# Performance work log

Measured on AMD Instinct MI355X. Metric: run time of the kernel, lower is better.

The kernel has to match this reference:

```python
import jax, jax.numpy as jnp
import numpy as np

B, T, I, H = 4096, 128, 32, 64


def _u(key, shape, bound):
    return jax.random.uniform(key, shape, jnp.float32, -bound, bound)


def setup_inputs() -> dict:
    key = jax.random.key(0)
    ks = jax.random.split(key, 14)
    bound = 1.0 / np.sqrt(H)  # torch LSTM/Linear default init scale
    inp = {
        "x": jax.random.normal(ks[0], (B, T, I), jnp.float32),
        "Wih0": _u(ks[1], (4 * H, I), bound),
        "Whh0": _u(ks[2], (4 * H, H), bound),
        "bih0": _u(ks[3], (4 * H,), bound),
        "bhh0": _u(ks[4], (4 * H,), bound),
        "Wih1": _u(ks[5], (4 * H, H), bound),
        "Whh1": _u(ks[6], (4 * H, H), bound),
        "bih1": _u(ks[7], (4 * H,), bound),
        "bhh1": _u(ks[8], (4 * H,), bound),
        "Wc1": _u(ks[9], (32, H), 1.0 / np.sqrt(H)),
        "bc1": _u(ks[10], (32,), 1.0 / np.sqrt(H)),
        "Wc2": _u(ks[11], (1, 32), 1.0 / np.sqrt(32)),
        "bc2": _u(ks[12], (1,), 1.0 / np.sqrt(32)),
    }
    return inp


def lstm_layer(x_tbi, Wih, Whh, bih, bhh):
    """x_tbi: [T, B, in]. Returns (all hidden [T,B,H], final hidden [B,H]).
    PyTorch gate order: i, f, g, o."""
    b = x_tbi.shape[1]
    h0 = jnp.zeros((b, Whh.shape[1]), x_tbi.dtype)
    c0 = jnp.zeros_like(h0)
    # precompute input projections for all timesteps in one big GEMM
    xproj = jnp.einsum('tbi,gi->tbg', x_tbi, Wih) + (bih + bhh)

    def step(carry, xp_t):
        h, c = carry
        gates = xp_t + h @ Whh.T  # [B, 4H]
        i, f, g, o = jnp.split(gates, 4, axis=-1)
        c = jax.nn.sigmoid(f) * c + jax.nn.sigmoid(i) * jnp.tanh(g)
        h = jax.nn.sigmoid(o) * jnp.tanh(c)
        return (h, c), h

    (hT, _), hs = jax.lax.scan(step, (h0, c0), xproj)
    return hs, hT


def reference(x, Wih0, Whh0, bih0, bhh0, Wih1, Whh1, bih1, bhh1, Wc1, bc1, Wc2, bc2):
    x_tbi = jnp.transpose(x, (1, 0, 2))  # [T, B, I]
    hs0, _ = lstm_layer(x_tbi, Wih0, Whh0, bih0, bhh0)
    # dropout between layers is identity in eval mode
    _, hT = lstm_layer(hs0, Wih1, Whh1, bih1, bhh1)  # h_n[-1]: [B, H]
    hidden = jax.nn.relu(hT @ Wc1.T + bc1)  # [B, 32]; classifier dropout = identity (eval)
    out = hidden @ Wc2.T + bc2  # [B, 1]
    return out.squeeze(-1)  # [B]
```

## Files before the change

kernel.cpp:

```cpp
#include <hip/hip_runtime.h>


#define TT 128
#define II 32
#define HH 64

typedef _Float16 half8 __attribute__((ext_vector_type(8)));
typedef float floatx4 __attribute__((ext_vector_type(4)));

#define LOG2E 1.4426950408889634f

__device__ __forceinline__ half8 load_w_frag(const float* __restrict__ W, int n, int K, int k0) {
    const float* p = W + (size_t)n * K + k0;
    float4 a = *(const float4*)p;
    float4 b = *(const float4*)(p + 4);
    half8 h;
    h[0] = (_Float16)a.x; h[1] = (_Float16)a.y; h[2] = (_Float16)a.z; h[3] = (_Float16)a.w;
    h[4] = (_Float16)b.x; h[5] = (_Float16)b.y; h[6] = (_Float16)b.z; h[7] = (_Float16)b.w;
    return h;
}

__device__ __forceinline__ float sig_tanh(float a, float b) {
    float bb = fminf(fmaxf(b, -15.f), 15.f);
    float u  = __builtin_amdgcn_exp2f(bb * (2.0f * LOG2E));
    float v  = __builtin_amdgcn_exp2f(-a * LOG2E);
    float num = u - 1.0f;
    float d1  = u + 1.0f;
    float den = fmaf(v, d1, d1);
    return num * __builtin_amdgcn_rcpf(den);
}

__device__ __forceinline__ float fsig(float x) {
    return __builtin_amdgcn_rcpf(1.0f + __builtin_amdgcn_exp2f(-x * LOG2E));
}

__global__ __launch_bounds__(512, 2) void lstm_fused(
    const float* __restrict__ x,
    const float* __restrict__ Wih0, const float* __restrict__ Whh0,
    const float* __restrict__ bih0, const float* __restrict__ bhh0,
    const float* __restrict__ Wih1, const float* __restrict__ Whh1,
    const float* __restrict__ bih1, const float* __restrict__ bhh1,
    const float* __restrict__ Wc1, const float* __restrict__ bc1,
    const float* __restrict__ Wc2, const float* __restrict__ bc2,
    float* __restrict__ out)
{
    __shared__ __align__(16) _Float16 xs[2][16][40];
    __shared__ __align__(16) _Float16 h0s[2][16][72];
    __shared__ __align__(16) _Float16 h1s[2][16][72];
    __shared__ __align__(16) float h1f[16][68];
    __shared__ float hid[16][32];

    const int tid  = threadIdx.x;
    const int wid  = tid >> 6;
    const int w4   = wid & 3;
    const bool isL0 = (wid < 4);
    const int lane = tid & 63;
    const int q  = lane >> 4;
    const int lr = lane & 15;
    const int b0 = blockIdx.x * 16;

    half8 bx0[4], bh0[4][2];
    half8 bi1[4][2], bh1[4][2];
    float biasv[4];
    if (isL0) {
        #pragma unroll
        for (int g = 0; g < 4; ++g) {
            int n = (w4 + 4 * g) * 16 + lr;
            bx0[g]    = load_w_frag(Wih0, n, 32, q * 8);
            bh0[g][0] = load_w_frag(Whh0, n, 64, q * 8);
            bh0[g][1] = load_w_frag(Whh0, n, 64, 32 + q * 8);
            biasv[g]  = bih0[n] + bhh0[n];
        }
    } else {
        #pragma unroll
        for (int g = 0; g < 4; ++g) {
            int n = (w4 + 4 * g) * 16 + lr;
            bi1[g][0] = load_w_frag(Wih1, n, 64, q * 8);
            bi1[g][1] = load_w_frag(Wih1, n, 64, 32 + q * 8);
            bh1[g][0] = load_w_frag(Whh1, n, 64, q * 8);
            bh1[g][1] = load_w_frag(Whh1, n, 64, 32 + q * 8);
            biasv[g]  = bih1[n] + bhh1[n];
        }
    }

    for (int i = tid; i < 2 * 16 * 72; i += 512) {
        ((_Float16*)h0s)[i] = (_Float16)0.0f;
        ((_Float16*)h1s)[i] = (_Float16)0.0f;
    }

    float cr[4] = {0.f, 0.f, 0.f, 0.f};

    const int xm = (tid >> 4) & 15;
    const int xf = (tid & 15) * 2;
    const float* xrow = x + ((size_t)(b0 + xm) * TT) * II + xf;
    float2 xbuf = {0.f, 0.f};
    if (isL0) {
        float2 x0 = *(const float2*)(xrow);
        xs[0][xm][xf]     = (_Float16)x0.x;
        xs[0][xm][xf + 1] = (_Float16)x0.y;
        if (TT > 1) xbuf = *(const float2*)(xrow + 1 * II);
    }

    for (int k = 0; k <= TT; ++k) {
        __syncthreads();

        const int rd = (k + 1) & 1;
        const int wr = k & 1;
        const bool doL0 = isL0 && (k < TT);
        const bool doL1 = (!isL0) && (k >= 1);
        float hnew[4];
        float2 xnew = xbuf;

        if (doL0) {
            half8 xfrag = *(const half8*)&xs[wr][lr][q * 8];
            half8 h0a   = *(const half8*)&h0s[rd][lr][q * 8];
            half8 h0b   = *(const half8*)&h0s[rd][lr][32 + q * 8];
            if (k + 2 < TT) xnew = *(const float2*)(xrow + (size_t)(k + 2) * II);
            floatx4 a0[4];
            #pragma unroll
            for (int g = 0; g < 4; ++g) {
                floatx4 acc = {biasv[g], biasv[g], biasv[g], biasv[g]};
                acc = __builtin_amdgcn_mfma_f32_16x16x32_f16(xfrag, bx0[g],    acc, 0, 0, 0);
                acc = __builtin_amdgcn_mfma_f32_16x16x32_f16(h0a,   bh0[g][0], acc, 0, 0, 0);
                acc = __builtin_amdgcn_mfma_f32_16x16x32_f16(h0b,   bh0[g][1], acc, 0, 0, 0);
                a0[g] = acc;
            }
            #pragma unroll
            for (int r = 0; r < 4; ++r) {
                float sf = fsig(a0[1][r]);
                float c  = fmaf(sf, cr[r], sig_tanh(a0[0][r], a0[2][r]));
                cr[r] = c;
                hnew[r] = sig_tanh(a0[3][r], c);
            }
        }
        if (doL1) {
            half8 g0a = *(const half8*)&h0s[rd][lr][q * 8];
            half8 g0b = *(const half8*)&h0s[rd][lr][32 + q * 8];
            half8 h1a = *(const half8*)&h1s[rd][lr][q * 8];
            half8 h1b = *(const half8*)&h1s[rd][lr][32 + q * 8];
            floatx4 a1[4];
            #pragma unroll
            for (int g = 0; g < 4; ++g) {
                floatx4 acc = {biasv[g], biasv[g], biasv[g], biasv[g]};
                acc = __builtin_amdgcn_mfma_f32_16x16x32_f16(g0a, bi1[g][0], acc, 0, 0, 0);
                acc = __builtin_amdgcn_mfma_f32_16x16x32_f16(g0b, bi1[g][1], acc, 0, 0, 0);
                acc = __builtin_amdgcn_mfma_f32_16x16x32_f16(h1a, bh1[g][0], acc, 0, 0, 0);
                acc = __builtin_amdgcn_mfma_f32_16x16x32_f16(h1b, bh1[g][1], acc, 0, 0, 0);
                a1[g] = acc;
            }
            #pragma unroll
            for (int r = 0; r < 4; ++r) {
                float sf = fsig(a1[1][r]);
                float c  = fmaf(sf, cr[r], sig_tanh(a1[0][r], a1[2][r]));
                cr[r] = c;
                hnew[r] = sig_tanh(a1[3][r], c);
            }
        }

        if (doL0) {
            #pragma unroll
            for (int r = 0; r < 4; ++r)
                h0s[wr][q * 4 + r][w4 * 16 + lr] = (_Float16)hnew[r];
            if (k + 1 < TT) {
                xs[rd][xm][xf]     = (_Float16)xbuf.x;
                xs[rd][xm][xf + 1] = (_Float16)xbuf.y;
            }
            xbuf = xnew;
        }
        if (doL1) {
            if (k == TT) {
                #pragma unroll
                for (int r = 0; r < 4; ++r)
                    h1f[q * 4 + r][w4 * 16 + lr] = hnew[r];
            } else {
                #pragma unroll
                for (int r = 0; r < 4; ++r)
                    h1s[wr][q * 4 + r][w4 * 16 + lr] = (_Float16)hnew[r];
            }
        }
    }
    __syncthreads();

    if (tid < 256) {
        int m = tid >> 4;
        int u = (tid & 15) * 2;
        float a = bc1[u], b = bc1[u + 1];
        const float* w0 = Wc1 + u * 64;
        const float* w1 = Wc1 + (u + 1) * 64;
        #pragma unroll 8
        for (int kk = 0; kk < 64; ++kk) {
            float hv = h1f[m][kk];
            a += hv * w0[kk];
            b += hv * w1[kk];
        }
        hid[m][u]     = fmaxf(a, 0.f);
        hid[m][u + 1] = fmaxf(b, 0.f);
    }
    __syncthreads();
    if (tid < 16) {
        float o = bc2[0];
        #pragma unroll
        for (int u = 0; u < 32; ++u) o += hid[tid][u] * Wc2[u];
        out[b0 + tid] = o;
    }
}

extern "C" void kernel_launch(void* const* d_in, const int* in_sizes, int n_in,
                              void* d_out, int out_size, void* d_ws, size_t ws_size,
                              hipStream_t stream) {
    (void)in_sizes; (void)n_in; (void)d_ws; (void)ws_size; (void)out_size;
    const float* x    = (const float*)d_in[0];
    const float* Wih0 = (const float*)d_in[1];
    const float* Whh0 = (const float*)d_in[2];
    const float* bih0 = (const float*)d_in[3];
    const float* bhh0 = (const float*)d_in[4];
    const float* Wih1 = (const float*)d_in[5];
    const float* Whh1 = (const float*)d_in[6];
    const float* bih1 = (const float*)d_in[7];
    const float* bhh1 = (const float*)d_in[8];
    const float* Wc1  = (const float*)d_in[9];
    const float* bc1  = (const float*)d_in[10];
    const float* Wc2  = (const float*)d_in[11];
    const float* bc2  = (const float*)d_in[12];
    lstm_fused<<<dim3(256), dim3(512), 0, stream>>>(
        x, Wih0, Whh0, bih0, bhh0, Wih1, Whh1, bih1, bhh1, Wc1, bc1, Wc2, bc2,
        (float*)d_out);
}
```

Before: 206.0 us.

## Load x fragments directly into registers per lane, drop shared x staging

```diff
diff --git a/kernel.cpp b/kernel.cpp
--- a/kernel.cpp
+++ b/kernel.cpp
@@ -20,16 +20,25 @@
     return h;
 }
 
-__device__ __forceinline__ float sig_tanh(float a, float b) {
-    float bb = fminf(fmaxf(b, -15.f), 15.f);
-    float u  = __builtin_amdgcn_exp2f(bb * (2.0f * LOG2E));
+__device__ __forceinline__ half8 cvt_frag(float4 a, float4 b) {
+    half8 h;
+    h[0] = (_Float16)a.x; h[1] = (_Float16)a.y; h[2] = (_Float16)a.z; h[3] = (_Float16)a.w;
+    h[4] = (_Float16)b.x; h[5] = (_Float16)b.y; h[6] = (_Float16)b.z; h[7] = (_Float16)b.w;
+    return h;
+}
+
+__device__ __forceinline__ float sig_tanh_nc(float a, float b) {
+    float u  = __builtin_amdgcn_exp2f(b * (2.0f * LOG2E));
     float v  = __builtin_amdgcn_exp2f(-a * LOG2E);
     float num = u - 1.0f;
     float d1  = u + 1.0f;
     float den = fmaf(v, d1, d1);
     return num * __builtin_amdgcn_rcpf(den);
 }
-
+__device__ __forceinline__ float sig_tanh_cl(float a, float b) {
+    float bb = fminf(fmaxf(b, -15.f), 15.f);
+    return sig_tanh_nc(a, bb);
+}
 __device__ __forceinline__ float fsig(float x) {
     return __builtin_amdgcn_rcpf(1.0f + __builtin_amdgcn_exp2f(-x * LOG2E));
 }
@@ -44,7 +53,6 @@
     const float* __restrict__ Wc2, const float* __restrict__ bc2,
     float* __restrict__ out)
 {
-    __shared__ __align__(16) _Float16 xs[2][16][40];
     __shared__ __align__(16) _Float16 h0s[2][16][72];
     __shared__ __align__(16) _Float16 h1s[2][16][72];
     __shared__ __align__(16) float h1f[16][68];
@@ -90,17 +98,18 @@
 
     float cr[4] = {0.f, 0.f, 0.f, 0.f};
 
-    const int xm = (tid >> 4) & 15;
-    const int xf = (tid & 15) * 2;
-    const float* xrow = x + ((size_t)(b0 + xm) * TT) * II + xf;
-    float2 xbuf = {0.f, 0.f};
+    const float* xlane = x + ((size_t)(b0 + lr) * TT) * II + q * 8;
+    half8 xfrag_cur;
+    float4 xra, xrb;
     if (isL0) {
-        float2 x0 = *(const float2*)(xrow);
-        xs[0][xm][xf]     = (_Float16)x0.x;
-        xs[0][xm][xf + 1] = (_Float16)x0.y;
-        if (TT > 1) xbuf = *(const float2*)(xrow + 1 * II);
-    }
-
+        float4 a0 = *(const float4*)(xlane);
+        float4 b0f = *(const float4*)(xlane + 4);
+        xfrag_cur = cvt_frag(a0, b0f);
+        xra = *(const float4*)(xlane + II);
+        xrb = *(const float4*)(xlane + II + 4);
+    }
+
+    #pragma unroll 2
     for (int k = 0; k <= TT; ++k) {
         __syncthreads();
 
@@ -109,28 +118,30 @@
         const bool doL0 = isL0 && (k < TT);
         const bool doL1 = (!isL0) && (k >= 1);
         float hnew[4];
-        float2 xnew = xbuf;
 
         if (doL0) {
-            half8 xfrag = *(const half8*)&xs[wr][lr][q * 8];
-            half8 h0a   = *(const half8*)&h0s[rd][lr][q * 8];
-            half8 h0b   = *(const half8*)&h0s[rd][lr][32 + q * 8];
-            if (k + 2 < TT) xnew = *(const float2*)(xrow + (size_t)(k + 2) * II);
+            half8 h0a = *(const half8*)&h0s[rd][lr][q * 8];
+            half8 h0b = *(const half8*)&h0s[rd][lr][32 + q * 8];
+            half8 xfrag_nxt = cvt_frag(xra, xrb);
+            int t2 = (k + 2 < TT) ? (k + 2) : (TT - 1);
+            xra = *(const float4*)(xlane + (size_t)t2 * II);
+            xrb = *(const float4*)(xlane + (size_t)t2 * II + 4);
             floatx4 a0[4];
             #pragma unroll
             for (int g = 0; g < 4; ++g) {
                 floatx4 acc = {biasv[g], biasv[g], biasv[g], biasv[g]};
-                acc = __builtin_amdgcn_mfma_f32_16x16x32_f16(xfrag, bx0[g],    acc, 0, 0, 0);
-                acc = __builtin_amdgcn_mfma_f32_16x16x32_f16(h0a,   bh0[g][0], acc, 0, 0, 0);
-                acc = __builtin_amdgcn_mfma_f32_16x16x32_f16(h0b,   bh0[g][1], acc, 0, 0, 0);
+                acc = __builtin_amdgcn_mfma_f32_16x16x32_f16(xfrag_cur, bx0[g],    acc, 0, 0, 0);
+                acc = __builtin_amdgcn_mfma_f32_16x16x32_f16(h0a,       bh0[g][0], acc, 0, 0, 0);
+                acc = __builtin_amdgcn_mfma_f32_16x16x32_f16(h0b,       bh0[g][1], acc, 0, 0, 0);
                 a0[g] = acc;
             }
+            xfrag_cur = xfrag_nxt;
             #pragma unroll
             for (int r = 0; r < 4; ++r) {
                 float sf = fsig(a0[1][r]);
-                float c  = fmaf(sf, cr[r], sig_tanh(a0[0][r], a0[2][r]));
+                float c  = fmaf(sf, cr[r], sig_tanh_nc(a0[0][r], a0[2][r]));
                 cr[r] = c;
-                hnew[r] = sig_tanh(a0[3][r], c);
+                hnew[r] = sig_tanh_cl(a0[3][r], c);
             }
         }
         if (doL1) {
@@ -151,9 +162,9 @@
             #pragma unroll
             for (int r = 0; r < 4; ++r) {
                 float sf = fsig(a1[1][r]);
-                float c  = fmaf(sf, cr[r], sig_tanh(a1[0][r], a1[2][r]));
+                float c  = fmaf(sf, cr[r], sig_tanh_nc(a1[0][r], a1[2][r]));
                 cr[r] = c;
-                hnew[r] = sig_tanh(a1[3][r], c);
+                hnew[r] = sig_tanh_cl(a1[3][r], c);
             }
         }
 
@@ -161,11 +172,6 @@
             #pragma unroll
             for (int r = 0; r < 4; ++r)
                 h0s[wr][q * 4 + r][w4 * 16 + lr] = (_Float16)hnew[r];
-            if (k + 1 < TT) {
-                xs[rd][xm][xf]     = (_Float16)xbuf.x;
-                xs[rd][xm][xf + 1] = (_Float16)xbuf.y;
-            }
-            xbuf = xnew;
         }
         if (doL1) {
             if (k == TT) {
```

After: 212.5 us. +3.1%, slower.
